# Performance work log

Measured on AMD Instinct MI355X. Metric: run time of the kernel, lower is better.

## Reference

```python
import jax, jax.numpy as jnp
import numpy as np

HEADS = 16


def setup_inputs() -> dict:
    key0 = jax.random.key(0)
    ks = jax.random.split(key0, 12)
    B, S, H = 4, 2048, 1024
    init = lambda k, shape: (jax.random.normal(k, shape, dtype=jnp.float32) * 0.02)
    return {
        "key": jax.random.normal(ks[0], (B, S, H), dtype=jnp.float32),
        "query": jax.random.normal(ks[1], (B, S, H), dtype=jnp.float32),
        "value": jax.random.normal(ks[2], (B, S, H), dtype=jnp.float32),
        "mask": jnp.zeros((B, 1, S, S), dtype=jnp.float32),  # additive mask
        "wq": init(ks[3], (H, H)), "bq": jnp.zeros((H,), jnp.float32),
        "wk": init(ks[4], (H, H)), "bk": jnp.zeros((H,), jnp.float32),
        "wv": init(ks[5], (H, H)), "bv": jnp.zeros((H,), jnp.float32),
        "wo": init(ks[6], (H, H)), "bo": jnp.zeros((H,), jnp.float32),
    }


def reference(key, query, value, mask, wq, bq, wk, bk, wv, bv, wo, bo):
    B, S, H = query.shape
    Hs = H // HEADS
    # Linear projections (torch Linear: x @ W^T + b), split heads -> [B, Hn, S, Hs]
    split = lambda x: x.reshape(B, S, HEADS, Hs).transpose(0, 2, 1, 3)
    q = split(query @ wq.T + bq)
    k = split(key @ wk.T + bk)
    v = split(value @ wv.T + bv)
    scale = 1.0 / jnp.sqrt(jnp.asarray(Hs, q.dtype))
    scores = jnp.einsum("bhqd,bhkd->bhqk", q, k) * scale  # [B, Hn, S, S]
    probs = jax.nn.softmax(scores + mask, axis=-1)  # dropout p=0 -> identity
    ctx = jnp.einsum("bhqk,bhkd->bhqd", probs, v)
    ctx = ctx.transpose(0, 2, 1, 3).reshape(B, S, H)
    return ctx @ wo.T + bo
```

## Files before the change

### kernel.cpp

```cpp
#include <hip/hip_runtime.h>
#include <hip/hip_bf16.h>

typedef __bf16 bf16;
typedef __bf16 bf16x4 __attribute__((ext_vector_type(4)));
typedef __bf16 bf16x8 __attribute__((ext_vector_type(8)));
typedef float f32x4 __attribute__((ext_vector_type(4)));
typedef float f32x16 __attribute__((ext_vector_type(16)));
typedef unsigned u32x4 __attribute__((ext_vector_type(4)));

#define MFMA16(a, b, c) __builtin_amdgcn_mfma_f32_16x16x32_bf16((a), (b), (c), 0, 0, 0)
#define MFMA32(a, b, c) __builtin_amdgcn_mfma_f32_32x32x16_bf16((a), (b), (c), 0, 0, 0)

__device__ __forceinline__ int xcd_swizzle(int bid, int nblk) {
  const int per = nblk >> 3;
  return (bid & 7) * per + (bid >> 3);
}

__device__ __forceinline__ void gload_lds16(const bf16* g, bf16* lds) {
  __builtin_amdgcn_global_load_lds(
      (const __attribute__((address_space(1))) void*)g,
      (__attribute__((address_space(3))) void*)lds, 16, 0, 0);
}

__device__ __forceinline__ unsigned pack2bf(float a, float b) {
  const unsigned short ua = __builtin_bit_cast(unsigned short, (bf16)a);
  const unsigned short ub = __builtin_bit_cast(unsigned short, (bf16)b);
  return (unsigned)ua | ((unsigned)ub << 16);
}

template <typename T> struct StageRegs;
template <> struct StageRegs<float> { float4 lo[4], hi[4]; };
template <> struct StageRegs<bf16> { bf16x8 v[4]; };

template <typename T>
__device__ __forceinline__ void stage_issue(StageRegs<T>& r, const T* base,
                                            int rowstride, int brc, int k0,
                                            int tid) {
#pragma unroll
  for (int i = 0; i < 4; ++i) {
    const int c = i * 256 + tid;
    const int row = c >> 3, lin = c & 7;
    const T* p = base + (size_t)(brc + row) * rowstride + k0 + lin * 8;
    if constexpr (sizeof(T) == 4) {
      r.lo[i] = *reinterpret_cast<const float4*>(p);
      r.hi[i] = *reinterpret_cast<const float4*>(p + 4);
    } else {
      r.v[i] = *reinterpret_cast<const bf16x8*>(p);
    }
  }
}

template <typename T>
__device__ __forceinline__ void stage_write(const StageRegs<T>& r, bf16* sm,
                                            int tid) {
#pragma unroll
  for (int i = 0; i < 4; ++i) {
    const int c = i * 256 + tid;
    const int row = c >> 3, lin = c & 7;
    const int slot = lin ^ (row & 7);
    bf16x8 v;
    if constexpr (sizeof(T) == 4) {
      const float4 a = r.lo[i], b = r.hi[i];
      v[0] = (bf16)a.x; v[1] = (bf16)a.y; v[2] = (bf16)a.z; v[3] = (bf16)a.w;
      v[4] = (bf16)b.x; v[5] = (bf16)b.y; v[6] = (bf16)b.z; v[7] = (bf16)b.w;
    } else {
      v = r.v[i];
    }
    *reinterpret_cast<bf16x8*>(sm + row * 64 + slot * 8) = v;
  }
}

template <typename TA>
__device__ __forceinline__ void gemm_core(const TA* A, const float* W,
                                          int brow, int bcol, int tid, int wm,
                                          int wn, int l15, int l4,
                                          bf16 (*Asm)[8192], bf16 (*Bsm)[8192],
                                          f32x4 (&acc)[4][4]) {
  StageRegs<TA> ra;
  StageRegs<float> rb;
  stage_issue(ra, A, 1024, brow, 0, tid);
  stage_issue(rb, W, 1024, bcol, 0, tid);
  int p = 0;
  for (int t = 0; t < 16; ++t) {
    stage_write(ra, Asm[p], tid);
    stage_write(rb, Bsm[p], tid);
    if (t + 1 < 16) {
      stage_issue(ra, A, 1024, brow, (t + 1) << 6, tid);
      stage_issue(rb, W, 1024, bcol, (t + 1) << 6, tid);
    }
    __syncthreads();
#pragma unroll
    for (int kk = 0; kk < 2; ++kk) {
      bf16x8 af[4], bfr[4];
#pragma unroll
      for (int m = 0; m < 4; ++m) {
        const int row = wm + m * 16 + l15;
        const int slot = (kk * 4 + l4) ^ (row & 7);
        af[m] = *reinterpret_cast<const bf16x8*>(Asm[p] + row * 64 + slot * 8);
      }
#pragma unroll
      for (int n = 0; n < 4; ++n) {
        const int row = wn + n * 16 + l15;
        const int slot = (kk * 4 + l4) ^ (row & 7);
        bfr[n] = *reinterpret_cast<const bf16x8*>(Bsm[p] + row * 64 + slot * 8);
      }
      __builtin_amdgcn_s_setprio(1);
#pragma unroll
      for (int m = 0; m < 4; ++m)
#pragma unroll
        for (int n = 0; n < 4; ++n)
          acc[m][n] = MFMA16(af[m], bfr[n], acc[m][n]);
      __builtin_amdgcn_s_setprio(0);
    }
    __syncthreads();
    p ^= 1;
  }
}

__global__ __launch_bounds__(256, 2) void qkv_gemm_kernel(
    const float* __restrict__ query, const float* __restrict__ key,
    const float* __restrict__ value, const float* __restrict__ wq,
    const float* __restrict__ wk, const float* __restrict__ wv,
    const float* __restrict__ bq, const float* __restrict__ bk,
    const float* __restrict__ bv, bf16* __restrict__ Qws,
    bf16* __restrict__ Kws, bf16* __restrict__ Vt, float qscale) {
  __shared__ bf16 Asm[2][128 * 64];
  __shared__ bf16 Bsm[2][128 * 64];
  const int tid = threadIdx.x;
  const int lane = tid & 63;
  const int wid = tid >> 6;
  const int l15 = lane & 15;
  const int l4 = lane >> 4;
  const int bid = xcd_swizzle(blockIdx.x, 1536);
  const int seg = bid / 512;
  const int inner = bid % 512;
  const int brow = (inner >> 3) << 7;
  const int bcol = (inner & 7) << 7;
  const int wm = (wid >> 1) << 6;
  const int wn = (wid & 1) << 6;

  const float* A = seg == 0 ? query : (seg == 1 ? key : value);
  const float* W = seg == 0 ? wq : (seg == 1 ? wk : wv);
  const float* bias = seg == 0 ? bq : (seg == 1 ? bk : bv);

  f32x4 acc[4][4] = {};
  gemm_core(A, W, brow, bcol, tid, wm, wn, l15, l4, Asm, Bsm, acc);

  const int r0 = brow + wm + l4 * 4;
  const int c0 = bcol + wn + l15;
  if (seg < 2) {
    bf16* C = seg == 0 ? Qws : Kws;
    const float cs = seg == 0 ? qscale : 1.0f;
#pragma unroll
    for (int n = 0; n < 4; ++n) {
      const float bvv = bias[c0 + n * 16];
#pragma unroll
      for (int m = 0; m < 4; ++m)
#pragma unroll
        for (int r = 0; r < 4; ++r)
          C[(size_t)(r0 + m * 16 + r) * 1024 + (c0 + n * 16)] =
              (bf16)((acc[m][n][r] + bvv) * cs);
    }
  } else {
#pragma unroll
    for (int n = 0; n < 4; ++n) {
      const float bvv = bias[c0 + n * 16];
      const int col = c0 + n * 16;
#pragma unroll
      for (int m = 0; m < 4; ++m) {
        const int row = r0 + m * 16;
        const int bq_ = row >> 11;
        const int srow = row & 2047;
        bf16x4 pk4;
#pragma unroll
        for (int r = 0; r < 4; ++r) pk4[r] = (bf16)(acc[m][n][r] + bvv);
        *reinterpret_cast<bf16x4*>(
            &Vt[(size_t)(bq_ * 1024 + col) * 2048 + srow]) = pk4;
      }
    }
  }
}

__global__ __launch_bounds__(256, 2) void out_gemm_kernel(
    const bf16* __restrict__ A, const float* __restrict__ W,
    const float* __restrict__ bias, float* __restrict__ C) {
  __shared__ bf16 Asm[2][128 * 64];
  __shared__ bf16 Bsm[2][128 * 64];
  const int tid = threadIdx.x;
  const int lane = tid & 63;
  const int wid = tid >> 6;
  const int l15 = lane & 15;
  const int l4 = lane >> 4;
  const int bid = xcd_swizzle(blockIdx.x, 512);
  const int brow = (bid >> 3) << 7;
  const int bcol = (bid & 7) << 7;
  const int wm = (wid >> 1) << 6;
  const int wn = (wid & 1) << 6;

  f32x4 acc[4][4] = {};
  gemm_core(A, W, brow, bcol, tid, wm, wn, l15, l4, Asm, Bsm, acc);

  const int r0 = brow + wm + l4 * 4;
  const int c0 = bcol + wn + l15;
#pragma unroll
  for (int n = 0; n < 4; ++n) {
    const float bvv = bias[c0 + n * 16];
#pragma unroll
    for (int m = 0; m < 4; ++m)
#pragma unroll
      for (int r = 0; r < 4; ++r)
        C[(size_t)(r0 + m * 16 + r) * 1024 + (c0 + n * 16)] =
            acc[m][n][r] + bvv;
  }
}

__global__ __launch_bounds__(256) void prep_mask_kernel(
    const float* __restrict__ mask, bf16* __restrict__ M2) {
  const float LOG2E = 1.44269504088896f;
  const int T0 = blockIdx.x * 256 + threadIdx.x;
#pragma unroll
  for (int i = 0; i < 4; ++i) {
    const int O = T0 + i * 524288;
    const int a = O & 3;
    const int h5 = (O >> 2) & 1;
    const int q = (O >> 3) & 2047;
    const int t = (O >> 14) & 31;
    const int b = O >> 19;
    const float* src = mask + ((size_t)(b * 2048 + q)) * 2048 + t * 64 +
                       32 * (a >> 1) + 16 * (a & 1) + 8 * h5;
    const float4 x = *reinterpret_cast<const float4*>(src);
    const float4 y = *reinterpret_cast<const float4*>(src + 4);
    bf16x8 v;
    v[0] = (bf16)(x.x * LOG2E); v[1] = (bf16)(x.y * LOG2E);
    v[2] = (bf16)(x.z * LOG2E); v[3] = (bf16)(x.w * LOG2E);
    v[4] = (bf16)(y.x * LOG2E); v[5] = (bf16)(y.y * LOG2E);
    v[6] = (bf16)(y.z * LOG2E); v[7] = (bf16)(y.w * LOG2E);
    *reinterpret_cast<bf16x8*>(&M2[(size_t)O * 8]) = v;
  }
}

__global__ __launch_bounds__(256, 3) void attn_kernel(
    const bf16* __restrict__ Q, const bf16* __restrict__ Kt,
    const bf16* __restrict__ Vt, const bf16* __restrict__ M2,
    bf16* __restrict__ ctx) {
  __shared__ bf16 Ksm[2][64 * 64];
  __shared__ bf16 Vsm[2][64 * 64];
  const int lid = xcd_swizzle(blockIdx.x, 1024);
  const int h = lid & 15;
  const int qb = (lid >> 4) & 15;
  const int b = lid >> 8;
  const int tid = threadIdx.x;
  const int lane = tid & 63;
  const int wid = tid >> 6;
  const int l31 = lane & 31;
  const int h5 = lane >> 5;
  const int qbase = qb * 128 + wid * 32;

  bf16x8 qf[4];
#pragma unroll
  for (int c = 0; c < 4; ++c)
    qf[c] = *reinterpret_cast<const bf16x8*>(
        &Q[(size_t)(b * 2048 + qbase + l31) * 1024 + h * 64 + c * 16 + h5 * 8]);

  f32x16 o[2] = {};
  float lrow = 0.f;

  const bf16* Kb = Kt + (size_t)b * 2048 * 1024 + h * 64;
  const bf16* Vb = Vt + (size_t)(b * 16 + h) * 64 * 2048;

  const int ca = tid, cb = 256 + tid;
  const int ra_ = ca >> 3, la = (ca & 7) ^ (ra_ & 7);
  const int rb_ = cb >> 3, lb = (cb & 7) ^ (rb_ & 7);
  const int pra = (ra_ & 51) | ((ra_ & 4) << 1) | ((ra_ & 8) >> 1);
  const int prb = (rb_ & 51) | ((rb_ & 4) << 1) | ((rb_ & 8) >> 1);
  const bf16* kga = Kb + (size_t)pra * 1024 + la * 8;
  const bf16* kgb = Kb + (size_t)prb * 1024 + lb * 8;
  const bf16* vga = Vb + (size_t)ra_ * 2048 + la * 8;
  const bf16* vgb = Vb + (size_t)rb_ * 2048 + lb * 8;
  const bf16* mp =
      M2 + ((size_t)(b * 32) * 2048 + qbase + l31) * 64 + h5 * 32;

  auto stage = [&](int p) {
    gload_lds16(kga, &Ksm[p][tid * 8]);
    gload_lds16(kgb, &Ksm[p][2048 + tid * 8]);
    gload_lds16(vga, &Vsm[p][tid * 8]);
    gload_lds16(vgb, &Vsm[p][2048 + tid * 8]);
    kga += 64 * 1024; kgb += 64 * 1024;
    vga += 64; vgb += 64;
  };
  u32x4 mA[4], mB[4];
  auto load_mask = [&](u32x4(&mr)[4]) {
#pragma unroll
    for (int i = 0; i < 4; ++i)
      mr[i] = *reinterpret_cast<const u32x4*>(mp + i * 8);
    mp += 2048 * 64;
  };

  auto tile_compute = [&](int p, u32x4(&mr)[4]) {
    f32x16 sf[2];
#pragma unroll
    for (int w = 0; w < 16; ++w) {
      const unsigned word = mr[w >> 2][w & 3];
      const int s = w >> 3;
      const int base = ((w >> 1) & 3) * 4 + (w & 1) * 2;
      sf[s][base + 0] = __builtin_bit_cast(float, word << 16);
      sf[s][base + 1] = __builtin_bit_cast(float, word & 0xffff0000u);
    }

    __builtin_amdgcn_s_setprio(1);
#pragma unroll
    for (int s = 0; s < 2; ++s) {
#pragma unroll
      for (int c = 0; c < 4; ++c) {
        const int row = s * 32 + l31;
        const int slot = (2 * c + h5) ^ (row & 7);
        const bf16x8 kf =
            *reinterpret_cast<const bf16x8*>(&Ksm[p][row * 64 + slot * 8]);
        sf[s] = MFMA32(kf, qf[c], sf[s]);
      }
    }
    __builtin_amdgcn_s_setprio(0);

    unsigned pk[2][4][2];
#pragma unroll
    for (int s = 0; s < 2; ++s) {
#pragma unroll
      for (int g = 0; g < 4; ++g) {
        const float p0 = __builtin_exp2f(sf[s][g * 4 + 0]);
        const float p1 = __builtin_exp2f(sf[s][g * 4 + 1]);
        const float p2 = __builtin_exp2f(sf[s][g * 4 + 2]);
        const float p3 = __builtin_exp2f(sf[s][g * 4 + 3]);
        lrow += (p0 + p1) + (p2 + p3);
        pk[s][g][0] = pack2bf(p0, p1);
        pk[s][g][1] = pack2bf(p2, p3);
      }
    }

    __builtin_amdgcn_s_setprio(1);
#pragma unroll
    for (int c = 0; c < 4; ++c) {
      const int s = c >> 1;
      const int g0 = 2 * (c & 1);
      const u32x4 uu = {pk[s][g0][0], pk[s][g0][1], pk[s][g0 + 1][0],
                        pk[s][g0 + 1][1]};
      const bf16x8 pa = __builtin_bit_cast(bf16x8, uu);
#pragma unroll
      for (int dsub = 0; dsub < 2; ++dsub) {
        const int row = dsub * 32 + l31;
        const int slot = (2 * c + h5) ^ (row & 7);
        const bf16x8 vf =
            *reinterpret_cast<const bf16x8*>(&Vsm[p][row * 64 + slot * 8]);
        o[dsub] = MFMA32(pa, vf, o[dsub]);
      }
    }
    __builtin_amdgcn_s_setprio(0);
  };

  stage(0);
  load_mask(mA);

  for (int t = 0; t < 32; t += 2) {
    if (t + 1 < 32) {
      stage(1);
      load_mask(mB);
      asm volatile("s_waitcnt vmcnt(8)" ::: "memory");
    } else {
      asm volatile("s_waitcnt vmcnt(0)" ::: "memory");
    }
    __builtin_amdgcn_s_barrier();
    __builtin_amdgcn_sched_barrier(0);
    tile_compute(0, mA);
    __builtin_amdgcn_s_barrier();
    if (t + 2 < 32) {
      stage(0);
      load_mask(mA);
      asm volatile("s_waitcnt vmcnt(8)" ::: "memory");
    } else {
      asm volatile("s_waitcnt vmcnt(0)" ::: "memory");
    }
    __builtin_amdgcn_s_barrier();
    __builtin_amdgcn_sched_barrier(0);
    tile_compute(1, mB);
    __builtin_amdgcn_s_barrier();
  }

  lrow += __shfl_xor(lrow, 32, 64);
  const float linv = __builtin_amdgcn_rcpf(lrow);
#pragma unroll
  for (int reg = 0; reg < 16; ++reg) {
    const int qr = (reg & 3) + 8 * (reg >> 2) + 4 * h5;
    const float li = __shfl(linv, qr, 64);
    const int q = qbase + qr;
#pragma unroll
    for (int dsub = 0; dsub < 2; ++dsub) {
      ctx[(size_t)(b * 2048 + q) * 1024 + h * 64 + dsub * 32 + l31] =
          (bf16)(o[dsub][reg] * li);
    }
  }
}

extern "C" void kernel_launch(void* const* d_in, const int* in_sizes, int n_in,
                              void* d_out, int out_size, void* d_ws,
                              size_t ws_size, hipStream_t stream) {
  const float* key = (const float*)d_in[0];
  const float* query = (const float*)d_in[1];
  const float* value = (const float*)d_in[2];
  const float* mask = (const float*)d_in[3];
  const float* wq = (const float*)d_in[4];
  const float* bq = (const float*)d_in[5];
  const float* wk = (const float*)d_in[6];
  const float* bk = (const float*)d_in[7];
  const float* wv = (const float*)d_in[8];
  const float* bv = (const float*)d_in[9];
  const float* wo = (const float*)d_in[10];
  const float* bo = (const float*)d_in[11];
  float* out = (float*)d_out;

  const size_t NBSH = (size_t)4 * 2048 * 1024;
  bf16* Qws = (bf16*)d_ws;
  bf16* Kws = Qws + NBSH;
  bf16* Vt = Kws + NBSH;
  bf16* M2 = (bf16*)d_out;

  const dim3 blk(256);
  prep_mask_kernel<<<2048, blk, 0, stream>>>(mask, M2);
  qkv_gemm_kernel<<<1536, blk, 0, stream>>>(query, key, value, wq, wk, wv, bq,
                                            bk, bv, Qws, Kws, Vt,
                                            0.18033688011112f);
  attn_kernel<<<1024, blk, 0, stream>>>(Qws, Kws, Vt, M2, Qws);
  out_gemm_kernel<<<512, blk, 0, stream>>>(Qws, wo, bo, out);
}
```

Measured before the change: 296.8 us.

## Use 512-thread attention blocks covering 256 queries, with inline-asm exp2 and bf16 pack

The attention kernel now runs 8 waves per block, each block covering 256 query rows, and launches half as many blocks. Each K/V tile staged in shared memory is therefore reused by twice as many waves, and each thread issues one load per tile instead of two; the vmcnt waits are adjusted to match. The softmax exp2 and bf16 packing are replaced by inline v_exp_f32 and v_cvt_pk_bf16_f32 instructions to cut ALU work. Larger blocks raise per-CU register pressure under the new launch bounds and leave fewer blocks to balance across CUs.

```diff
diff --git a/kernel.cpp b/kernel.cpp
--- a/kernel.cpp
+++ b/kernel.cpp
@@ -22,10 +22,16 @@
       (__attribute__((address_space(3))) void*)lds, 16, 0, 0);
 }
 
-__device__ __forceinline__ unsigned pack2bf(float a, float b) {
-  const unsigned short ua = __builtin_bit_cast(unsigned short, (bf16)a);
-  const unsigned short ub = __builtin_bit_cast(unsigned short, (bf16)b);
-  return (unsigned)ua | ((unsigned)ub << 16);
+__device__ __forceinline__ float fast_exp2(float x) {
+  float r;
+  asm("v_exp_f32 %0, %1\n\ts_nop 1" : "=v"(r) : "v"(x));
+  return r;
+}
+
+__device__ __forceinline__ unsigned cvt_pk_bf16(float lo, float hi) {
+  unsigned r;
+  asm("v_cvt_pk_bf16_f32 %0, %1, %2" : "=v"(r) : "v"(lo), "v"(hi));
+  return r;
 }
 
 template <typename T> struct StageRegs;
@@ -239,22 +245,22 @@
   }
 }
 
-__global__ __launch_bounds__(256, 3) void attn_kernel(
+__global__ __launch_bounds__(512, 4) void attn_kernel(
     const bf16* __restrict__ Q, const bf16* __restrict__ Kt,
     const bf16* __restrict__ Vt, const bf16* __restrict__ M2,
     bf16* __restrict__ ctx) {
   __shared__ bf16 Ksm[2][64 * 64];
   __shared__ bf16 Vsm[2][64 * 64];
-  const int lid = xcd_swizzle(blockIdx.x, 1024);
+  const int lid = xcd_swizzle(blockIdx.x, 512);
   const int h = lid & 15;
-  const int qb = (lid >> 4) & 15;
-  const int b = lid >> 8;
+  const int qb = (lid >> 4) & 7;
+  const int b = lid >> 7;
   const int tid = threadIdx.x;
   const int lane = tid & 63;
   const int wid = tid >> 6;
   const int l31 = lane & 31;
   const int h5 = lane >> 5;
-  const int qbase = qb * 128 + wid * 32;
+  const int qbase = qb * 256 + wid * 32;
 
   bf16x8 qf[4];
 #pragma unroll
@@ -268,25 +274,18 @@
   const bf16* Kb = Kt + (size_t)b * 2048 * 1024 + h * 64;
   const bf16* Vb = Vt + (size_t)(b * 16 + h) * 64 * 2048;
 
-  const int ca = tid, cb = 256 + tid;
-  const int ra_ = ca >> 3, la = (ca & 7) ^ (ra_ & 7);
-  const int rb_ = cb >> 3, lb = (cb & 7) ^ (rb_ & 7);
-  const int pra = (ra_ & 51) | ((ra_ & 4) << 1) | ((ra_ & 8) >> 1);
-  const int prb = (rb_ & 51) | ((rb_ & 4) << 1) | ((rb_ & 8) >> 1);
-  const bf16* kga = Kb + (size_t)pra * 1024 + la * 8;
-  const bf16* kgb = Kb + (size_t)prb * 1024 + lb * 8;
-  const bf16* vga = Vb + (size_t)ra_ * 2048 + la * 8;
-  const bf16* vgb = Vb + (size_t)rb_ * 2048 + lb * 8;
+  const int row_ = tid >> 3, lin_ = (tid & 7) ^ (row_ & 7);
+  const int prow = (row_ & 51) | ((row_ & 4) << 1) | ((row_ & 8) >> 1);
+  const bf16* kga = Kb + (size_t)prow * 1024 + lin_ * 8;
+  const bf16* vga = Vb + (size_t)row_ * 2048 + lin_ * 8;
   const bf16* mp =
       M2 + ((size_t)(b * 32) * 2048 + qbase + l31) * 64 + h5 * 32;
 
   auto stage = [&](int p) {
     gload_lds16(kga, &Ksm[p][tid * 8]);
-    gload_lds16(kgb, &Ksm[p][2048 + tid * 8]);
     gload_lds16(vga, &Vsm[p][tid * 8]);
-    gload_lds16(vgb, &Vsm[p][2048 + tid * 8]);
-    kga += 64 * 1024; kgb += 64 * 1024;
-    vga += 64; vgb += 64;
+    kga += 64 * 1024;
+    vga += 64;
   };
   u32x4 mA[4], mB[4];
   auto load_mask = [&](u32x4(&mr)[4]) {
@@ -326,13 +325,13 @@
     for (int s = 0; s < 2; ++s) {
 #pragma unroll
       for (int g = 0; g < 4; ++g) {
-        const float p0 = __builtin_exp2f(sf[s][g * 4 + 0]);
-        const float p1 = __builtin_exp2f(sf[s][g * 4 + 1]);
-        const float p2 = __builtin_exp2f(sf[s][g * 4 + 2]);
-        const float p3 = __builtin_exp2f(sf[s][g * 4 + 3]);
+        const float p0 = fast_exp2(sf[s][g * 4 + 0]);
+        const float p1 = fast_exp2(sf[s][g * 4 + 1]);
+        const float p2 = fast_exp2(sf[s][g * 4 + 2]);
+        const float p3 = fast_exp2(sf[s][g * 4 + 3]);
         lrow += (p0 + p1) + (p2 + p3);
-        pk[s][g][0] = pack2bf(p0, p1);
-        pk[s][g][1] = pack2bf(p2, p3);
+        pk[s][g][0] = cvt_pk_bf16(p0, p1);
+        pk[s][g][1] = cvt_pk_bf16(p2, p3);
       }
     }
 
@@ -363,7 +362,7 @@
     if (t + 1 < 32) {
       stage(1);
       load_mask(mB);
-      asm volatile("s_waitcnt vmcnt(8)" ::: "memory");
+      asm volatile("s_waitcnt vmcnt(6)" ::: "memory");
     } else {
       asm volatile("s_waitcnt vmcnt(0)" ::: "memory");
     }
@@ -374,7 +373,7 @@
     if (t + 2 < 32) {
       stage(0);
       load_mask(mA);
-      asm volatile("s_waitcnt vmcnt(8)" ::: "memory");
+      asm volatile("s_waitcnt vmcnt(6)" ::: "memory");
     } else {
       asm volatile("s_waitcnt vmcnt(0)" ::: "memory");
     }
@@ -422,11 +421,10 @@
   bf16* Vt = Kws + NBSH;
   bf16* M2 = (bf16*)d_out;
 
-  const dim3 blk(256);
-  prep_mask_kernel<<<2048, blk, 0, stream>>>(mask, M2);
-  qkv_gemm_kernel<<<1536, blk, 0, stream>>>(query, key, value, wq, wk, wv, bq,
-                                            bk, bv, Qws, Kws, Vt,
-                                            0.18033688011112f);
-  attn_kernel<<<1024, blk, 0, stream>>>(Qws, Kws, Vt, M2, Qws);
-  out_gemm_kernel<<<512, blk, 0, stream>>>(Qws, wo, bo, out);
-}
+  prep_mask_kernel<<<2048, dim3(256), 0, stream>>>(mask, M2);
+  qkv_gemm_kernel<<<1536, dim3(256), 0, stream>>>(query, key, value, wq, wk,
+                                                  wv, bq, bk, bv, Qws, Kws, Vt,
+                                                  0.18033688011112f);
+  attn_kernel<<<512, dim3(512), 0, stream>>>(Qws, Kws, Vt, M2, Qws);
+  out_gemm_kernel<<<512, dim3(256), 0, stream>>>(Qws, wo, bo, out);
+}
```

After: 334.9 us. 12.8% more time.
